# Performance work log

Measured on AMD Instinct MI355X. Metric: run time of the kernel, lower is better.

## Reference

```python
import jax, jax.numpy as jnp
import numpy as np

EPS = 1e-6

def _ln2d(x, w, b):
    # LayerNorm2d: normalize over channel dim per pixel
    mu = x.mean(axis=1, keepdims=True)
    var = ((x - mu) ** 2).mean(axis=1, keepdims=True)
    return (x - mu) / jnp.sqrt(var + EPS) * w[None, :, None, None] + b[None, :, None, None]

def _conv1x1(x, w, b):
    return jnp.einsum('oc,bchw->bohw', w, x) + b[None, :, None, None]

def setup_inputs() -> dict:
    key = jax.random.key(0)
    ks = jax.random.split(key, 20)
    B, c, H, W = 4, 32, 256, 256
    dw = 2 * c
    k, wH, wW = 3, 32, 32
    s = 0.05
    d = {}
    d['inp'] = jax.random.normal(ks[0], (B, c, H, W), jnp.float32)
    d['conv2_weight'] = jax.random.normal(ks[1], (B, dw, k, k, wH, wW), jnp.float32) * 0.1
    d['conv1_w'] = jax.random.normal(ks[2], (dw, c), jnp.float32) * s
    d['conv1_b'] = jnp.zeros((dw,), jnp.float32)
    d['conv3_w'] = jax.random.normal(ks[3], (c, c), jnp.float32) * s
    d['conv3_b'] = jnp.zeros((c,), jnp.float32)
    d['sca_w'] = jax.random.normal(ks[4], (c, c), jnp.float32) * s
    d['sca_b'] = jnp.zeros((c,), jnp.float32)
    d['conv4_w'] = jax.random.normal(ks[5], (dw, c), jnp.float32) * s
    d['conv4_b'] = jnp.zeros((dw,), jnp.float32)
    d['conv5_w'] = jax.random.normal(ks[6], (c, c), jnp.float32) * s
    d['conv5_b'] = jnp.zeros((c,), jnp.float32)
    d['norm1_w'] = jnp.ones((c,), jnp.float32)
    d['norm1_b'] = jnp.zeros((c,), jnp.float32)
    d['norm2_w'] = jnp.ones((c,), jnp.float32)
    d['norm2_b'] = jnp.zeros((c,), jnp.float32)
    # original inits these to zero; use small random so the block is non-trivial
    d['beta'] = jax.random.normal(ks[7], (1, c, 1, 1), jnp.float32) * 0.1
    d['gamma'] = jax.random.normal(ks[8], (1, c, 1, 1), jnp.float32) * 0.1
    return d

def reference(inp, conv2_weight, conv1_w, conv1_b, conv3_w, conv3_b, sca_w, sca_b,
              conv4_w, conv4_b, conv5_w, conv5_b, norm1_w, norm1_b, norm2_w, norm2_b,
              beta, gamma):
    B, c, H, W = inp.shape
    x = _ln2d(inp, norm1_w, norm1_b)
    x = _conv1x1(x, conv1_w, conv1_b)                 # [B, 2c, H, W]
    Bw, C, kH, kW, wH, wW = conv2_weight.shape
    # bilinear upsample (half-pixel centers, == torch align_corners=False)
    w2 = conv2_weight.reshape(B * C, kH * kW, wH, wW)
    w2 = jax.image.resize(w2, (B * C, kH * kW, H, W), method='linear')
    w2 = w2.reshape(B, C, kH * kW, H, W)
    # ddf with all-ones channel filter + 'mul' == per-pixel spatial 3x3 conv per channel
    pad = kH // 2
    xp = jnp.pad(x, ((0, 0), (0, 0), (pad, pad), (pad, pad)))
    patches = jnp.stack([xp[:, :, i:i + H, j:j + W]
                         for i in range(kH) for j in range(kW)], axis=2)  # [B,2c,9,H,W]
    x = (patches * w2).sum(axis=2)                    # [B, 2c, H, W]
    x1, x2 = jnp.split(x, 2, axis=1)                  # SimpleGate
    x = x1 * x2                                       # [B, c, H, W]
    s = _conv1x1(x.mean(axis=(2, 3), keepdims=True), sca_w, sca_b)
    x = x * s
    x = _conv1x1(x, conv3_w, conv3_b)
    y = inp + x * beta
    x = _conv1x1(_ln2d(y, norm2_w, norm2_b), conv4_w, conv4_b)
    x1, x2 = jnp.split(x, 2, axis=1)
    x = _conv1x1(x1 * x2, conv5_w, conv5_b)
    return y + x * gamma
```

## Files before the change

### kernel.cpp

```cpp
#include <hip/hip_runtime.h>
#include <hip/hip_bf16.h>

typedef __hip_bfloat16 bf16;
typedef __attribute__((ext_vector_type(8))) unsigned short u16x8;
typedef __attribute__((ext_vector_type(8))) short s16x8;
typedef __attribute__((ext_vector_type(4))) float f32x4;
typedef __attribute__((ext_vector_type(4))) unsigned short us16x4;

#define B_   4
#define C_   32
#define DW_  64
#define H_   256
#define W_   256
#define P_   65536
#define SRC_ 32
#define TRS_ 272
#define TPL_ 70176

#define OW1    0
#define OB1    2048
#define OW3    2112
#define OB3    3136
#define OWS    3168
#define OBS    4192
#define OW4    4224
#define OB4    6272
#define OW5    6336
#define OB5    7360
#define ON1W   7392
#define ON1B   7424
#define ON2W   7456
#define ON2B   7488
#define OBETA  7520
#define OGAMMA 7552
#define OSUMS  7584
#define OSVEC  7712
#define OFLAG  7900
#define CWF_BOFF 32768ull
#define T1_BOFF  (CWF_BOFF + 9437184ull)
#define G_BOFF   (T1_BOFF + 35930112ull)

__device__ __forceinline__ bf16  f2b(float v){ return __float2bfloat16(v); }
__device__ __forceinline__ float bfu(unsigned short u){ return __uint_as_float(((unsigned int)u) << 16); }
__device__ __forceinline__ unsigned short fbits(float v){
    bf16 b = __float2bfloat16(v);
    return *reinterpret_cast<unsigned short*>(&b);
}

template<typename T> __device__ __forceinline__ float ldf(const T* p);
template<> __device__ __forceinline__ float ldf<float>(const float* p){ return *p; }
template<> __device__ __forceinline__ float ldf<bf16>(const bf16* p){ return __bfloat162float(*p); }

template<typename T> struct dtag;
template<> struct dtag<float>{ static constexpr int v = 0; };
template<> struct dtag<bf16>{ static constexpr int v = 1; };

__device__ __forceinline__ f32x4 MF(s16x8 a, s16x8 b, f32x4 c){
    return __builtin_amdgcn_mfma_f32_16x16x32_bf16(a, b, c, 0, 0, 0);
}
__device__ __forceinline__ s16x8 wfrag8(const float* p){
    float4 a = *(const float4*)p;
    float4 c = *(const float4*)(p + 4);
    s16x8 r;
    r[0] = (short)fbits(a.x); r[1] = (short)fbits(a.y);
    r[2] = (short)fbits(a.z); r[3] = (short)fbits(a.w);
    r[4] = (short)fbits(c.x); r[5] = (short)fbits(c.y);
    r[6] = (short)fbits(c.z); r[7] = (short)fbits(c.w);
    return r;
}

__global__ void k_detect(const unsigned short* __restrict__ raw, int* __restrict__ flag)
{
    int t = threadIdx.x;
    int bad = 0;
    for (int k = 0; k < 8; ++k) {
        unsigned short u = raw[2 * (t + 64 * k)];
        float v = __uint_as_float(((unsigned int)u) << 16);
        if (!(fabsf(v) < 1e6f)) bad = 1;
    }
    int anybad = __any(bad);
    if (t == 0) *flag = anybad ? 0 : 1;
}

template<typename T>
__global__ void k_prep(const T* __restrict__ w1, const T* __restrict__ b1,
                       const T* __restrict__ w3, const T* __restrict__ b3,
                       const T* __restrict__ wsc, const T* __restrict__ bsc_,
                       const T* __restrict__ w4, const T* __restrict__ b4,
                       const T* __restrict__ w5, const T* __restrict__ b5,
                       const T* __restrict__ n1w, const T* __restrict__ n1b,
                       const T* __restrict__ n2w, const T* __restrict__ n2b,
                       const T* __restrict__ bet, const T* __restrict__ gam,
                       float* __restrict__ wsf, const int* __restrict__ flag)
{
    if (*flag != dtag<T>::v) return;
    int t = threadIdx.x;
    for (int i = t; i < 2048; i += 256) wsf[OW1 + i] = ldf<T>(w1 + i);
    for (int i = t; i < 64;   i += 256) wsf[OB1 + i] = ldf<T>(b1 + i);
    for (int i = t; i < 1024; i += 256) wsf[OW3 + i] = ldf<T>(w3 + i);
    for (int i = t; i < 32;   i += 256) wsf[OB3 + i] = ldf<T>(b3 + i);
    for (int i = t; i < 1024; i += 256) wsf[OWS + i] = ldf<T>(wsc + i);
    for (int i = t; i < 32;   i += 256) wsf[OBS + i] = ldf<T>(bsc_ + i);
    for (int i = t; i < 2048; i += 256) wsf[OW4 + i] = ldf<T>(w4 + i);
    for (int i = t; i < 64;   i += 256) wsf[OB4 + i] = ldf<T>(b4 + i);
    for (int i = t; i < 1024; i += 256) wsf[OW5 + i] = ldf<T>(w5 + i);
    for (int i = t; i < 32;   i += 256) wsf[OB5 + i] = ldf<T>(b5 + i);
    for (int i = t; i < 32;   i += 256) wsf[ON1W + i] = ldf<T>(n1w + i);
    for (int i = t; i < 32;   i += 256) wsf[ON1B + i] = ldf<T>(n1b + i);
    for (int i = t; i < 32;   i += 256) wsf[ON2W + i] = ldf<T>(n2w + i);
    for (int i = t; i < 32;   i += 256) wsf[ON2B + i] = ldf<T>(n2b + i);
    for (int i = t; i < 32;   i += 256) wsf[OBETA + i] = ldf<T>(bet + i);
    for (int i = t; i < 32;   i += 256) wsf[OGAMMA + i] = ldf<T>(gam + i);
    for (int i = t; i < 128;  i += 256) wsf[OSUMS + i] = 0.f;
}

__global__ void k_cwf(const void* __restrict__ cw, float4* __restrict__ cwf4,
                      const int* __restrict__ flag)
{
    int i4 = blockIdx.x * 256 + threadIdx.x;
    if (*flag == 0) {
        cwf4[i4] = ((const float4*)cw)[i4];
    } else {
        const ushort4* p = (const ushort4*)cw;
        ushort4 v = p[i4];
        cwf4[i4] = make_float4(bfu(v.x), bfu(v.y), bfu(v.z), bfu(v.w));
    }
}

#define OSTR1_ 280
template<typename T>
__device__ __forceinline__ void ln1_body(const T* __restrict__ inp,
        const float* __restrict__ wsf, bf16* __restrict__ t1p,
        short* __restrict__ xsh, short* __restrict__ osh)
{
    const int t = threadIdx.x;
    const int b = blockIdx.x >> 8;
    const int h = blockIdx.x & 255;
    const int p0 = h << 8;

    {
        const T* ip = inp + (size_t)(b * C_) * P_ + p0 + t;
        float v[C_];
        float m = 0.f;
        #pragma unroll
        for (int ch = 0; ch < C_; ++ch) { v[ch] = ldf<T>(ip + (size_t)ch * P_); m += v[ch]; }
        m *= (1.f / C_);
        float var = 0.f;
        #pragma unroll
        for (int ch = 0; ch < C_; ++ch) { float d = v[ch] - m; var += d * d; }
        var *= (1.f / C_);
        float inv = rsqrtf(var + 1e-6f);
        u16x8* xr = (u16x8*)(xsh + t * 32);
        #pragma unroll
        for (int qq = 0; qq < 4; ++qq) {
            u16x8 vv;
            #pragma unroll
            for (int j = 0; j < 8; ++j) {
                int ch = qq * 8 + j;
                vv[j] = fbits((v[ch] - m) * inv * wsf[ON1W + ch] + wsf[ON1B + ch]);
            }
            xr[qq] = vv;
        }
        int och = t >> 4, cc = t & 15;
        osh[och * OSTR1_ + (cc == 0 ? 0 : 256 + cc)] = 0;
    }
    __syncthreads();

    const int lane = t & 63, wv = t >> 6;
    const int l15 = lane & 15, l4 = lane >> 4;
    const int wp0 = wv * 64;

    s16x8 w1f[4];
    f32x4 b1v[4];
    #pragma unroll
    for (int m = 0; m < 4; ++m) {
        w1f[m] = wfrag8(wsf + OW1 + (m * 16 + l15) * 32 + l4 * 8);
        b1v[m] = *(const f32x4*)(wsf + OB1 + m * 16 + l4 * 4);
    }
    s16x8 xb[4];
    #pragma unroll
    for (int tn = 0; tn < 4; ++tn)
        xb[tn] = *(const s16x8*)(xsh + (wp0 + tn * 16 + l15) * 32 + l4 * 8);

    const size_t prow = (size_t)(b * DW_) * TPL_ + (size_t)(h + 1) * TRS_;
    #pragma unroll
    for (int m = 0; m < 4; ++m) {
        #pragma unroll
        for (int tn = 0; tn < 4; ++tn) {
            f32x4 acc = MF(w1f[m], xb[tn], b1v[m]);
            int px = wp0 + tn * 16 + l15;
            #pragma unroll
            for (int i = 0; i < 4; ++i)
                osh[(l4 * 4 + i) * OSTR1_ + 1 + px] = (short)fbits(acc[i]);
        }
        __syncthreads();
        for (int it = 0; it < 3; ++it) {
            int idx = it * 256 + t;
            if (idx < 544) {
                int och = idx / 34, ck = idx - och * 34;
                u16x8 v = *(const u16x8*)(osh + och * OSTR1_ + ck * 8);
                *(u16x8*)((unsigned short*)t1p + prow + (size_t)(m * 16 + och) * TPL_ + ck * 8) = v;
            }
        }
        __syncthreads();
    }

    if (h == 0 || h == 255) {
        size_t rbase = (size_t)(b * DW_) * TPL_ + (h == 0 ? 0 : (size_t)257 * TRS_);
        u16x8 z;
        #pragma unroll
        for (int j = 0; j < 8; ++j) z[j] = 0;
        for (int it = 0; it < 9; ++it) {
            int idx = it * 256 + t;
            if (idx < 2176) {
                int och = idx / 34, ck = idx - och * 34;
                *(u16x8*)((unsigned short*)t1p + rbase + (size_t)och * TPL_ + ck * 8) = z;
            }
        }
    }
}

__global__ __launch_bounds__(256, 4) void k_ln1_conv1(const void* __restrict__ inp,
        const float* __restrict__ wsf, bf16* __restrict__ t1p,
        const int* __restrict__ flag)
{
    __shared__ short xsh[256 * 32];
    __shared__ short osh[16 * OSTR1_];
    if (*flag == 0) ln1_body<float>((const float*)inp, wsf, t1p, xsh, osh);
    else            ln1_body<bf16>((const bf16*)inp, wsf, t1p, xsh, osh);
}

#define G_ 4
__global__ __launch_bounds__(256, 4) void k_ddf(const unsigned short* __restrict__ t1u,
        const float* __restrict__ cwf, bf16* __restrict__ g, float* __restrict__ sums)
{
    __shared__ float CWs[4320];

    int bid = blockIdx.x;
    int tile = bid & 31;
    int cg  = (bid >> 5) & 7;
    int b   = bid >> 8;
    int th = tile >> 2, tw = tile & 3;
    int cellh0 = th * 4;
    int cellw0 = tw * 8;
    int cp0 = cg * G_;

    {
        const float* cb = cwf + (size_t)b * (DW_ * 9 * 1024);
        for (int it = 0; it < 17; ++it) {
            int idx = it * 256 + threadIdx.x;
            if (idx < 4320) {
                int cc  = idx % 10;
                int t2  = idx / 10;
                int rr  = t2 % 6;
                int t3  = t2 / 6;
                int tap = t3 % 9;
                int chl = t3 / 9;
                int ch = (chl < G_) ? (cp0 + chl) : (C_ + cp0 + chl - G_);
                int cr = cellh0 - 1 + rr; cr = cr < 0 ? 0 : (cr > 31 ? 31 : cr);
                int cw = cellw0 - 1 + cc; cw = cw < 0 ? 0 : (cw > 31 ? 31 : cw);
                CWs[idx] = cb[ch * 9216 + tap * 1024 + cr * SRC_ + cw];
            }
        }
    }
    __syncthreads();

    int lane = threadIdx.x & 63, wid = threadIdx.x >> 6;
    int k = lane >> 3, r = lane & 7;
    int cellh = cellh0 + wid;
    int h = cellh * 8 + r;
    int w = (cellw0 + k) * 8;

    int rsel = r >> 2;
    float fh = rsel ? ((float)r * 0.125f - 0.4375f) : ((float)r * 0.125f + 0.5625f);
    float gh = 1.f - fh;
    int rr0k = (wid + rsel) * 10 + k;

    const unsigned short* tb = t1u + (size_t)(b * DW_) * TPL_ + (size_t)h * TRS_ + w;
    bf16* gp = g + (size_t)(b * C_) * P_ + h * 256 + w;

    for (int l = 0; l < G_; ++l) {
        int cp = cp0 + l;
        const unsigned short* pl1 = tb + (size_t)cp * TPL_;
        const unsigned short* pl2 = pl1 + (size_t)C_ * TPL_;
        const float* q1 = CWs + l * 540;
        const float* q2 = CWs + (G_ + l) * 540;

        float acc1[8], acc2[8];
        #pragma unroll
        for (int pass = 0; pass < 2; ++pass) {
            const unsigned short* pl = pass ? pl2 : pl1;
            const float* q = pass ? q2 : q1;
            float* acc = pass ? acc2 : acc1;

            u16x8 v8[3];
            unsigned int ve[3];
            #pragma unroll
            for (int i = 0; i < 3; ++i) {
                const unsigned short* rp = pl + i * TRS_;
                v8[i] = *(const u16x8*)rp;
                ve[i] = *(const unsigned int*)(rp + 8);
            }
            float S00[8], S01[8], S10[8], S11[8];
            #pragma unroll
            for (int c = 0; c < 8; ++c) { S00[c]=0.f; S01[c]=0.f; S10[c]=0.f; S11[c]=0.f; }
            #pragma unroll
            for (int i = 0; i < 3; ++i) {
                float p[10];
                #pragma unroll
                for (int j = 0; j < 8; ++j) p[j] = bfu((unsigned short)v8[i][j]);
                p[8] = bfu((unsigned short)(ve[i] & 0xFFFFu));
                p[9] = bfu((unsigned short)(ve[i] >> 16));
                #pragma unroll
                for (int j = 0; j < 3; ++j) {
                    const float* qb = q + (i * 3 + j) * 60 + rr0k;
                    float w00 = qb[0],  w01 = qb[1],  w02 = qb[2];
                    float w10 = qb[10], w11 = qb[11], w12 = qb[12];
                    #pragma unroll
                    for (int c = 0; c < 8; ++c) {
                        float pv = p[c + j];
                        S00[c] += pv * ((c < 4) ? w00 : w01);
                        S01[c] += pv * ((c < 4) ? w01 : w02);
                        S10[c] += pv * ((c < 4) ? w10 : w11);
                        S11[c] += pv * ((c < 4) ? w11 : w12);
                    }
                }
            }
            const float fwt[8] = {0.5625f, 0.6875f, 0.8125f, 0.9375f,
                                  0.0625f, 0.1875f, 0.3125f, 0.4375f};
            #pragma unroll
            for (int c = 0; c < 8; ++c) {
                float fw = fwt[c], gw = 1.f - fw;
                acc[c] = gh * (gw * S00[c] + fw * S01[c]) + fh * (gw * S10[c] + fw * S11[c]);
            }
        }

        u16x8 ov;
        float s = 0.f;
        #pragma unroll
        for (int c = 0; c < 8; ++c) {
            float gv = acc1[c] * acc2[c];
            s += gv;
            bf16 bv = f2b(gv);
            ov[c] = *reinterpret_cast<unsigned short*>(&bv);
        }
        *(u16x8*)(gp + (size_t)cp * P_) = ov;

        #pragma unroll
        for (int off = 32; off >= 1; off >>= 1) s += __shfl_xor(s, off, 64);
        if (lane == 0) atomicAdd(&sums[b * C_ + cp], s);
    }
}

#define XSTR_ 32
#define ISTR_ 33
#define OSTRT_ 260

template<typename T>
__device__ __forceinline__ void tail_body(const T* __restrict__ inp,
        const bf16* __restrict__ g, const float* __restrict__ wsf,
        T* __restrict__ out, short* __restrict__ xsh, float* __restrict__ ipsh,
        float* __restrict__ svsh)
{
    const int t = threadIdx.x;
    const int b = blockIdx.x >> 8;
    const int p0 = (blockIdx.x & 255) << 8;

    if (t < 32) {
        float acc = wsf[OBS + t];
        #pragma unroll
        for (int ch = 0; ch < C_; ++ch)
            acc += wsf[OWS + t * C_ + ch] * (wsf[OSUMS + b * C_ + ch] * (1.f / (float)P_));
        svsh[t] = acc;
    }
    __syncthreads();

    {
        const unsigned short* gp = (const unsigned short*)g + (size_t)(b * C_) * P_ + p0 + t;
        unsigned short row[32];
        #pragma unroll
        for (int ch = 0; ch < C_; ++ch)
            row[ch] = fbits(bfu(gp[(size_t)ch * P_]) * svsh[ch]);
        u16x8* xr = (u16x8*)(xsh + t * XSTR_);
        #pragma unroll
        for (int qq = 0; qq < 4; ++qq) {
            u16x8 vv;
            #pragma unroll
            for (int j = 0; j < 8; ++j) vv[j] = row[qq * 8 + j];
            xr[qq] = vv;
        }
        const T* ip = inp + (size_t)(b * C_) * P_ + p0 + t;
        float* ir = ipsh + t * ISTR_;
        #pragma unroll
        for (int ch = 0; ch < C_; ++ch)
            ir[ch] = ldf<T>(ip + (size_t)ch * P_);
    }
    __syncthreads();

    const int lane = t & 63, wv = t >> 6;
    const int l15 = lane & 15, l4 = lane >> 4;
    const int wp0 = wv * 64;

    s16x8 w3f[2], w4f[4];
    #pragma unroll
    for (int m = 0; m < 2; ++m) w3f[m] = wfrag8(wsf + OW3 + (m * 16 + l15) * 32 + l4 * 8);
    #pragma unroll
    for (int m = 0; m < 4; ++m) w4f[m] = wfrag8(wsf + OW4 + (m * 16 + l15) * 32 + l4 * 8);

    f32x4 y[2][4];
    {
        f32x4 b3v[2], btv[2];
        #pragma unroll
        for (int m = 0; m < 2; ++m) {
            b3v[m] = *(const f32x4*)(wsf + OB3   + m * 16 + l4 * 4);
            btv[m] = *(const f32x4*)(wsf + OBETA + m * 16 + l4 * 4);
        }
        #pragma unroll
        for (int tn = 0; tn < 4; ++tn) {
            int px = wp0 + tn * 16 + l15;
            s16x8 xb = *(const s16x8*)(xsh + px * XSTR_ + l4 * 8);
            const float* irr = ipsh + px * ISTR_ + l4 * 4;
            #pragma unroll
            for (int m = 0; m < 2; ++m) {
                f32x4 acc = MF(w3f[m], xb, b3v[m]);
                f32x4 yy;
                #pragma unroll
                for (int i = 0; i < 4; ++i)
                    yy[i] = irr[m * 16 + i] + acc[i] * btv[m][i];
                y[m][tn] = yy;
            }
        }
    }
    __syncthreads();

    {
        f32x4 nwv[2], nbv[2];
        #pragma unroll
        for (int m = 0; m < 2; ++m) {
            nwv[m] = *(const f32x4*)(wsf + ON2W + m * 16 + l4 * 4);
            nbv[m] = *(const f32x4*)(wsf + ON2B + m * 16 + l4 * 4);
        }
        #pragma unroll
        for (int tn = 0; tn < 4; ++tn) {
            float s = 0.f;
            #pragma unroll
            for (int m = 0; m < 2; ++m)
                #pragma unroll
                for (int i = 0; i < 4; ++i) s += y[m][tn][i];
            s += __shfl_xor(s, 16);
            s += __shfl_xor(s, 32);
            float mean = s * (1.f / 32.f);
            float q = 0.f;
            #pragma unroll
            for (int m = 0; m < 2; ++m)
                #pragma unroll
                for (int i = 0; i < 4; ++i) { float d = y[m][tn][i] - mean; q += d * d; }
            q += __shfl_xor(q, 16);
            q += __shfl_xor(q, 32);
            float inv = rsqrtf(q * (1.f / 32.f) + 1e-6f);
            int px = wp0 + tn * 16 + l15;
            #pragma unroll
            for (int m = 0; m < 2; ++m) {
                us16x4 pk;
                #pragma unroll
                for (int i = 0; i < 4; ++i)
                    pk[i] = fbits((y[m][tn][i] - mean) * inv * nwv[m][i] + nbv[m][i]);
                *(us16x4*)(xsh + px * XSTR_ + m * 16 + l4 * 4) = pk;
            }
        }
    }

    {
        f32x4 b4v[4];
        #pragma unroll
        for (int m = 0; m < 4; ++m)
            b4v[m] = *(const f32x4*)(wsf + OB4 + m * 16 + l4 * 4);
        s16x8 yb[4];
        #pragma unroll
        for (int tn = 0; tn < 4; ++tn)
            yb[tn] = *(const s16x8*)(xsh + (wp0 + tn * 16 + l15) * XSTR_ + l4 * 8);
        #pragma unroll
        for (int tn = 0; tn < 4; ++tn) {
            f32x4 a4[4];
            #pragma unroll
            for (int m = 0; m < 4; ++m) a4[m] = MF(w4f[m], yb[tn], b4v[m]);
            int px = wp0 + tn * 16 + l15;
            #pragma unroll
            for (int m = 0; m < 2; ++m) {
                us16x4 pk;
                #pragma unroll
                for (int i = 0; i < 4; ++i) pk[i] = fbits(a4[m][i] * a4[m + 2][i]);
                *(us16x4*)(xsh + px * XSTR_ + m * 16 + l4 * 4) = pk;
            }
        }
    }

    {
        s16x8 w5f[2];
        #pragma unroll
        for (int m = 0; m < 2; ++m) w5f[m] = wfrag8(wsf + OW5 + (m * 16 + l15) * 32 + l4 * 8);
        f32x4 b5v[2], gmv[2];
        #pragma unroll
        for (int m = 0; m < 2; ++m) {
            b5v[m] = *(const f32x4*)(wsf + OB5    + m * 16 + l4 * 4);
            gmv[m] = *(const f32x4*)(wsf + OGAMMA + m * 16 + l4 * 4);
        }
        s16x8 ub[4];
        #pragma unroll
        for (int tn = 0; tn < 4; ++tn)
            ub[tn] = *(const s16x8*)(xsh + (wp0 + tn * 16 + l15) * XSTR_ + l4 * 8);
        float* oshf = ipsh;
        #pragma unroll
        for (int tn = 0; tn < 4; ++tn) {
            int px = wp0 + tn * 16 + l15;
            #pragma unroll
            for (int m = 0; m < 2; ++m) {
                f32x4 acc = MF(w5f[m], ub[tn], b5v[m]);
                #pragma unroll
                for (int i = 0; i < 4; ++i)
                    oshf[(m * 16 + l4 * 4 + i) * OSTRT_ + px] = y[m][tn][i] + acc[i] * gmv[m][i];
            }
        }
    }
    __syncthreads();

    {
        const float* oshf = ipsh;
        if (dtag<T>::v == 0) {
            float* of = (float*)out;
            #pragma unroll
            for (int it = 0; it < 8; ++it) {
                int idx = it * 256 + t;
                int och = idx >> 6, ck = idx & 63;
                f32x4 v = *(const f32x4*)(oshf + och * OSTRT_ + ck * 4);
                *(f32x4*)(of + (size_t)(b * C_ + och) * P_ + p0 + ck * 4) = v;
            }
        } else {
            unsigned short* ob = (unsigned short*)out;
            #pragma unroll
            for (int it = 0; it < 4; ++it) {
                int idx = it * 256 + t;
                int och = idx >> 5, ck = idx & 31;
                f32x4 a = *(const f32x4*)(oshf + och * OSTRT_ + ck * 8);
                f32x4 c = *(const f32x4*)(oshf + och * OSTRT_ + ck * 8 + 4);
                u16x8 pk;
                pk[0] = fbits(a[0]); pk[1] = fbits(a[1]); pk[2] = fbits(a[2]); pk[3] = fbits(a[3]);
                pk[4] = fbits(c[0]); pk[5] = fbits(c[1]); pk[6] = fbits(c[2]); pk[7] = fbits(c[3]);
                *(u16x8*)(ob + (size_t)(b * C_ + och) * P_ + p0 + ck * 8) = pk;
            }
        }
    }
}

__global__ __launch_bounds__(256, 3) void k_tail(const void* __restrict__ inp,
        const bf16* __restrict__ g, const float* __restrict__ wsf,
        void* __restrict__ out, const int* __restrict__ flag)
{
    __shared__ short xsh[256 * XSTR_];
    __shared__ float ipsh[256 * ISTR_];
    __shared__ float svsh[32];
    if (*flag == 0) tail_body<float>((const float*)inp, g, wsf, (float*)out, xsh, ipsh, svsh);
    else            tail_body<bf16>((const bf16*)inp, g, wsf, (bf16*)out, xsh, ipsh, svsh);
}

extern "C" void kernel_launch(void* const* d_in, const int* in_sizes, int n_in,
                              void* d_out, int out_size, void* d_ws, size_t ws_size,
                              hipStream_t stream)
{
    float* wsf = (float*)d_ws;
    char* wsb = (char*)d_ws;
    float* cwf = (float*)(wsb + CWF_BOFF);
    bf16* t1p = (bf16*)(wsb + T1_BOFF);
    bf16* g   = (bf16*)(wsb + G_BOFF);
    int* flag = (int*)(wsf + OFLAG);

    k_detect<<<1, 64, 0, stream>>>((const unsigned short*)d_in[0], flag);

    int nblk = (B_ * P_) / 256;

    k_prep<float><<<1, 256, 0, stream>>>(
        (const float*)d_in[2], (const float*)d_in[3], (const float*)d_in[4],
        (const float*)d_in[5], (const float*)d_in[6], (const float*)d_in[7],
        (const float*)d_in[8], (const float*)d_in[9], (const float*)d_in[10],
        (const float*)d_in[11], (const float*)d_in[12], (const float*)d_in[13],
        (const float*)d_in[14], (const float*)d_in[15], (const float*)d_in[16],
        (const float*)d_in[17], wsf, flag);
    k_prep<bf16><<<1, 256, 0, stream>>>(
        (const bf16*)d_in[2], (const bf16*)d_in[3], (const bf16*)d_in[4],
        (const bf16*)d_in[5], (const bf16*)d_in[6], (const bf16*)d_in[7],
        (const bf16*)d_in[8], (const bf16*)d_in[9], (const bf16*)d_in[10],
        (const bf16*)d_in[11], (const bf16*)d_in[12], (const bf16*)d_in[13],
        (const bf16*)d_in[14], (const bf16*)d_in[15], (const bf16*)d_in[16],
        (const bf16*)d_in[17], wsf, flag);

    k_cwf<<<2304, 256, 0, stream>>>(d_in[1], (float4*)cwf, flag);

    k_ln1_conv1<<<nblk, 256, 0, stream>>>(d_in[0], wsf, t1p, flag);

    k_ddf<<<1024, 256, 0, stream>>>((const unsigned short*)t1p, cwf, g, wsf + OSUMS);

    k_tail<<<nblk, 256, 0, stream>>>(d_in[0], g, wsf, d_out, flag);
}
```

Before: 232.0 us.

## Transpose conv2 weights to cell-major layout and stage t1 tiles in LDS

k_cwf now transposes the low-resolution conv2 weights into a cell-major layout with taps and permuted channels innermost. This lets k_ddf gather its per-block weight halo with contiguous 8-channel runs instead of strided per-channel reads. k_ddf also stages each channel pair's t1 tile, including the halo, into shared memory before the 3x3 compute, replacing direct global loads of overlapping rows. The cost is an extra transpose pass, more LDS use and two added block barriers per channel.

```diff
diff --git a/kernel.cpp b/kernel.cpp
--- a/kernel.cpp
+++ b/kernel.cpp
@@ -114,16 +114,32 @@
     for (int i = t; i < 128;  i += 256) wsf[OSUMS + i] = 0.f;
 }
 
-__global__ void k_cwf(const void* __restrict__ cw, float4* __restrict__ cwf4,
-                      const int* __restrict__ flag)
-{
-    int i4 = blockIdx.x * 256 + threadIdx.x;
-    if (*flag == 0) {
-        cwf4[i4] = ((const float4*)cw)[i4];
-    } else {
-        const ushort4* p = (const ushort4*)cw;
-        ushort4 v = p[i4];
-        cwf4[i4] = make_float4(bfu(v.x), bfu(v.y), bfu(v.z), bfu(v.w));
+__global__ __launch_bounds__(256) void k_cwf(const void* __restrict__ cw,
+        float* __restrict__ cwfT, const int* __restrict__ flag)
+{
+    __shared__ float tile[64][65];
+    int blk = blockIdx.x;
+    int rct = blk & 15;
+    int tap = (blk >> 4) % 9;
+    int b   = blk / 144;
+    int rc0 = rct * 64;
+    int tl  = threadIdx.x & 63;
+    int tg  = threadIdx.x >> 6;
+    int fl  = *flag;
+    #pragma unroll
+    for (int it = 0; it < 16; ++it) {
+        int oc = it * 4 + tg;
+        size_t iidx = ((size_t)(b * DW_ + oc) * 9 + tap) * 1024 + rc0 + tl;
+        tile[oc][tl] = (fl == 0) ? ((const float*)cw)[iidx]
+                                 : bfu(((const unsigned short*)cw)[iidx]);
+    }
+    __syncthreads();
+    #pragma unroll
+    for (int it = 0; it < 16; ++it) {
+        int rcl = it * 4 + tg;
+        int p = tl;
+        int oc = ((p >> 2) & 1) * 32 + (p >> 3) * 4 + (p & 3);
+        cwfT[((size_t)(b * 1024 + rc0 + rcl) * 9 + tap) * 64 + p] = tile[oc][rcl];
     }
 }
 
@@ -232,9 +248,10 @@
 
 #define G_ 4
 __global__ __launch_bounds__(256, 4) void k_ddf(const unsigned short* __restrict__ t1u,
-        const float* __restrict__ cwf, bf16* __restrict__ g, float* __restrict__ sums)
+        const float* __restrict__ cwfT, bf16* __restrict__ g, float* __restrict__ sums)
 {
     __shared__ float CWs[4320];
+    __shared__ unsigned short Ts[4896];
 
     int bid = blockIdx.x;
     int tile = bid & 31;
@@ -246,58 +263,72 @@
     int cp0 = cg * G_;
 
     {
-        const float* cb = cwf + (size_t)b * (DW_ * 9 * 1024);
+        const float* cb = cwfT + (size_t)b * 589824;
         for (int it = 0; it < 17; ++it) {
             int idx = it * 256 + threadIdx.x;
             if (idx < 4320) {
-                int cc  = idx % 10;
-                int t2  = idx / 10;
-                int rr  = t2 % 6;
-                int t3  = t2 / 6;
-                int tap = t3 % 9;
-                int chl = t3 / 9;
-                int ch = (chl < G_) ? (cp0 + chl) : (C_ + cp0 + chl - G_);
+                int chp  = idx & 7;
+                int rest = idx >> 3;
+                int cc  = rest % 10;
+                int t3  = rest / 10;
+                int rr  = t3 % 6;
+                int tap = t3 / 6;
                 int cr = cellh0 - 1 + rr; cr = cr < 0 ? 0 : (cr > 31 ? 31 : cr);
                 int cw = cellw0 - 1 + cc; cw = cw < 0 ? 0 : (cw > 31 ? 31 : cw);
-                CWs[idx] = cb[ch * 9216 + tap * 1024 + cr * SRC_ + cw];
-            }
-        }
-    }
-    __syncthreads();
+                CWs[rest * 8 + chp] =
+                    cb[(size_t)(cr * 32 + cw) * 576 + tap * 64 + cg * 8 + chp];
+            }
+        }
+    }
 
     int lane = threadIdx.x & 63, wid = threadIdx.x >> 6;
     int k = lane >> 3, r = lane & 7;
-    int cellh = cellh0 + wid;
-    int h = cellh * 8 + r;
-    int w = (cellw0 + k) * 8;
+    int h0 = cellh0 * 8;
+    int w0 = cellw0 * 8;
+    int lrow = wid * 8 + r;
+    int h = h0 + lrow;
+    int w = w0 + k * 8;
 
     int rsel = r >> 2;
     float fh = rsel ? ((float)r * 0.125f - 0.4375f) : ((float)r * 0.125f + 0.5625f);
     float gh = 1.f - fh;
     int rr0k = (wid + rsel) * 10 + k;
 
-    const unsigned short* tb = t1u + (size_t)(b * DW_) * TPL_ + (size_t)h * TRS_ + w;
+    const unsigned short* gbase = t1u + (size_t)(b * DW_) * TPL_ + (size_t)h0 * TRS_ + w0;
     bf16* gp = g + (size_t)(b * C_) * P_ + h * 256 + w;
+
+    const float fwt[8] = {0.5625f, 0.6875f, 0.8125f, 0.9375f,
+                          0.0625f, 0.1875f, 0.3125f, 0.4375f};
 
     for (int l = 0; l < G_; ++l) {
         int cp = cp0 + l;
-        const unsigned short* pl1 = tb + (size_t)cp * TPL_;
-        const unsigned short* pl2 = pl1 + (size_t)C_ * TPL_;
-        const float* q1 = CWs + l * 540;
-        const float* q2 = CWs + (G_ + l) * 540;
+        __syncthreads();
+        for (int it = 0; it < 3; ++it) {
+            int idx = it * 256 + threadIdx.x;
+            if (idx < 612) {
+                int ps = idx >= 306 ? 1 : 0;
+                int rem = idx - ps * 306;
+                int row = rem / 9;
+                int ck = rem - row * 9;
+                const unsigned short* src = gbase + (size_t)(cp + ps * C_) * TPL_
+                                            + row * TRS_ + ck * 8;
+                *(u16x8*)(Ts + ps * 2448 + row * 72 + ck * 8) = *(const u16x8*)src;
+            }
+        }
+        __syncthreads();
 
         float acc1[8], acc2[8];
         #pragma unroll
         for (int pass = 0; pass < 2; ++pass) {
-            const unsigned short* pl = pass ? pl2 : pl1;
-            const float* q = pass ? q2 : q1;
+            const unsigned short* pl = Ts + pass * 2448;
             float* acc = pass ? acc2 : acc1;
+            int ch = pass ? (G_ + l) : l;
 
             u16x8 v8[3];
             unsigned int ve[3];
             #pragma unroll
             for (int i = 0; i < 3; ++i) {
-                const unsigned short* rp = pl + i * TRS_;
+                const unsigned short* rp = pl + (lrow + i) * 72 + k * 8;
                 v8[i] = *(const u16x8*)rp;
                 ve[i] = *(const unsigned int*)(rp + 8);
             }
@@ -313,9 +344,9 @@
                 p[9] = bfu((unsigned short)(ve[i] >> 16));
                 #pragma unroll
                 for (int j = 0; j < 3; ++j) {
-                    const float* qb = q + (i * 3 + j) * 60 + rr0k;
-                    float w00 = qb[0],  w01 = qb[1],  w02 = qb[2];
-                    float w10 = qb[10], w11 = qb[11], w12 = qb[12];
+                    const float* qb = CWs + ((i * 3 + j) * 60 + rr0k) * 8 + ch;
+                    float w00 = qb[0],  w01 = qb[8],  w02 = qb[16];
+                    float w10 = qb[80], w11 = qb[88], w12 = qb[96];
                     #pragma unroll
                     for (int c = 0; c < 8; ++c) {
                         float pv = p[c + j];
@@ -326,8 +357,6 @@
                     }
                 }
             }
-            const float fwt[8] = {0.5625f, 0.6875f, 0.8125f, 0.9375f,
-                                  0.0625f, 0.1875f, 0.3125f, 0.4375f};
             #pragma unroll
             for (int c = 0; c < 8; ++c) {
                 float fw = fwt[c], gw = 1.f - fw;
@@ -593,7 +622,7 @@
         (const bf16*)d_in[14], (const bf16*)d_in[15], (const bf16*)d_in[16],
         (const bf16*)d_in[17], wsf, flag);
 
-    k_cwf<<<2304, 256, 0, stream>>>(d_in[1], (float4*)cwf, flag);
+    k_cwf<<<576, 256, 0, stream>>>(d_in[1], cwf, flag);
 
     k_ln1_conv1<<<nblk, 256, 0, stream>>>(d_in[0], wsf, t1p, flag);
 
```

After: 243.0 us. +4.7%, slower.
